# Optimization experiments

Measured on AMD Instinct MI355X. Metric: run time of the kernel, lower is better.

Reference implementation:

```python
import jax, jax.numpy as jnp
import numpy as np

# DeepSeek V4 MLA sparse attention dims
T = 512            # query tokens
H = 64             # attention heads (SUPPORTED_HEAD_COUNTS)
KV_LORA = 512      # kv_lora_rank (value dim = latent nope part)
ROPE = 64          # qk_rope_head_dim
D = KV_LORA + ROPE # 576 = head_dim (matches alignment=576 in cache spec)
N_KV = 8192        # cached compressed-KV tokens
TOPK = 1024        # top-k selected tokens per query
SCALE = 1.0 / np.sqrt(D).astype(np.float32)


def setup_inputs() -> dict:
    key = jax.random.key(0)
    k1, k2, k3, k4 = jax.random.split(key, 4)
    q = jax.random.normal(k1, (T, H, D), dtype=jnp.float32)
    kv = jax.random.normal(k2, (N_KV, D), dtype=jnp.float32)   # compressed KV latent cache (1 kv head)
    topk_idx = jax.random.randint(k3, (T, TOPK), 0, N_KV, dtype=jnp.int32)
    sink = jax.random.normal(k4, (H,), dtype=jnp.float32)       # per-head attention sink logit
    return {"q": q, "kv": kv, "topk_idx": topk_idx, "sink": sink}


def reference(q, kv, topk_idx, sink):
    # Sparse MLA: each query token attends only to its top-k latent cache slots.
    valid = topk_idx >= 0                       # invalid slots marked negative
    idx = jnp.maximum(topk_idx, 0)
    g = kv[idx]                                  # [T, K, D] gathered latents
    # scores over gathered subset: [T, H, K]
    scores = jnp.einsum('thd,tkd->thk', q, g) * SCALE
    scores = jnp.where(valid[:, None, :], scores, -jnp.inf)
    # sink-aware softmax: sink acts as an extra logit with zero value
    m = jnp.maximum(jnp.max(scores, axis=-1), sink[None, :])   # [T, H]
    p = jnp.exp(scores - m[..., None])                          # [T, H, K]
    denom = jnp.sum(p, axis=-1) + jnp.exp(sink[None, :] - m)    # [T, H]
    # value = nope part (first KV_LORA dims) of latent -> output [T, H, KV_LORA]
    out = jnp.einsum('thk,tkv->thv', p, g[..., :KV_LORA]) / denom[..., None]
    return out
```

## Files before the change

### kernel.cpp

```cpp
#include <hip/hip_runtime.h>
#include <hip/hip_bf16.h>

#define T_TOK 512
#define NH    64
#define HD    576
#define DVAL  512
#define NKV   8192
#define TOPK  1024
#define KT    32
#define NITER (TOPK / KT)
#define KSTEPS (HD / 32)
#define SCALE 0.041666666666666664f
#define LOG2E 1.4426950408889634f
#define QSCL  (SCALE * LOG2E)
#define MFIX  8.0f
#define MB    (MFIX * LOG2E)

typedef __attribute__((ext_vector_type(4))) float f32x4;
typedef __attribute__((ext_vector_type(8))) _Float16 half8;
typedef __attribute__((ext_vector_type(4))) unsigned short us4;
typedef __attribute__((ext_vector_type(8))) unsigned short us8;
typedef __attribute__((ext_vector_type(4))) int i32x4;

__device__ __forceinline__ unsigned short f2h(float x) {
    _Float16 h = (_Float16)x;
    return __builtin_bit_cast(unsigned short, h);
}

__device__ __forceinline__ float fexp2(float x) {
#if __has_builtin(__builtin_amdgcn_exp2f)
    return __builtin_amdgcn_exp2f(x);
#else
    return __expf(x * 0.6931471805599453f);
#endif
}

template<int CTRL>
__device__ __forceinline__ float dppmv(float x) {
    int r = __builtin_amdgcn_update_dpp(0, __builtin_bit_cast(int, x), CTRL, 0xF, 0xF, true);
    return __builtin_bit_cast(float, r);
}
__device__ __forceinline__ float red16sum(float x) {
    x += dppmv<0xB1>(x);
    x += dppmv<0x4E>(x);
    x += dppmv<0x141>(x);
    x += dppmv<0x140>(x);
    return x;
}

#define TICK_BARRIER() do {                                   \
    asm volatile("s_waitcnt lgkmcnt(0)" ::: "memory");        \
    __builtin_amdgcn_s_barrier();                             \
    asm volatile("" ::: "memory");                            \
} while (0)

__global__ void cvt_kv_f16(const float* __restrict__ kv, unsigned short* __restrict__ kvb) {
    int i = blockIdx.x * 256 + threadIdx.x;
    const f32x4* src = (const f32x4*)kv + (size_t)i * 2;
    f32x4 a = src[0];
    f32x4 b = src[1];
    us8 w;
    w[0]=f2h(a[0]); w[1]=f2h(a[1]); w[2]=f2h(a[2]); w[3]=f2h(a[3]);
    w[4]=f2h(b[0]); w[5]=f2h(b[1]); w[6]=f2h(b[2]); w[7]=f2h(b[3]);
    ((us8*)kvb)[i] = w;
}

#define G_LD  584
#define P_LD  40
#define GT_IDX(row,key) (((((row) << 5) | (key))) ^ ((((row) >> 2) & 7) << 3))

struct StageRegs { us8 v[4]; us4 rope; };

__device__ __forceinline__ void stage_load(
    const unsigned short* __restrict__ kvb, const int* __restrict__ tkrow,
    int it, int w8, int kg, int lm, int quad, int l16, StageRegs& R)
{
    const int* ip = tkrow + it * KT + kg * 4;
    i32x4 r4 = *(const i32x4*)ip;
    int d0 = w8 * 64 + lm * 8;
    #pragma unroll
    for (int j = 0; j < 4; j++) {
        int r = r4[j] < 0 ? 0 : r4[j];
        R.v[j] = *(const us8*)(kvb + (size_t)r * HD + d0);
    }
    int kr = tkrow[it * KT + w8 * 4 + quad];
    if (kr < 0) kr = 0;
    R.rope = *(const us4*)(kvb + (size_t)kr * HD + 512 + l16 * 4);
}

__device__ __forceinline__ void stage_write(
    int w8, int kg, int lm, int quad, int l16, const StageRegs& R,
    unsigned short (*gp)[G_LD], unsigned short* gtp)
{
    int d0 = w8 * 64 + lm * 8;
    #pragma unroll
    for (int j = 0; j < 4; j++)
        *(us8*)&gp[kg * 4 + j][d0] = R.v[j];
    #pragma unroll
    for (int e = 0; e < 8; e++) {
        us4 wv;
        wv[0] = R.v[0][e]; wv[1] = R.v[1][e]; wv[2] = R.v[2][e]; wv[3] = R.v[3][e];
        *(us4*)&gtp[GT_IDX(d0 + e, kg * 4)] = wv;
    }
    *(us4*)&gp[w8 * 4 + quad][512 + l16 * 4] = R.rope;
}

__global__ __launch_bounds__(1024, 4) void mla_sparse_kernel(
    const float* __restrict__ q, const int* __restrict__ topk,
    const float* __restrict__ sink, const unsigned short* __restrict__ kvb,
    float* __restrict__ out)
{
    __shared__ unsigned short g2[2][KT][G_LD];
    __shared__ unsigned short gtb[2][DVAL * KT];
    __shared__ unsigned short pbuf[2][NH][P_LD];
    __shared__ float lhalf[2][NH];

    const int t    = blockIdx.x;
    const int tid  = threadIdx.x;
    const int lane = tid & 63;
    const int quad = lane >> 4;
    const int l16  = lane & 15;
    const int wave = __builtin_amdgcn_readfirstlane(tid >> 6);
    const int* tkrow = topk + (size_t)t * TOPK;

    if (wave < 8) {
        const int hg = wave >> 1;
        const int kh = wave & 1;
        const int qo = quad * 8;
        const int krow0 = kh * 16;
        half8 qf[KSTEPS];
        {
            const float* qrow = q + ((size_t)t * NH + (hg * 16 + l16)) * HD;
            #pragma unroll
            for (int ks = 0; ks < KSTEPS; ks++) {
                int d0 = ks * 32 + qo;
                f32x4 a = *(const f32x4*)(qrow + d0);
                f32x4 b = *(const f32x4*)(qrow + d0 + 4);
                half8 h;
                h[0]=(_Float16)(a[0]*QSCL); h[1]=(_Float16)(a[1]*QSCL);
                h[2]=(_Float16)(a[2]*QSCL); h[3]=(_Float16)(a[3]*QSCL);
                h[4]=(_Float16)(b[0]*QSCL); h[5]=(_Float16)(b[1]*QSCL);
                h[6]=(_Float16)(b[2]*QSCL); h[7]=(_Float16)(b[3]*QSCL);
                qf[ks] = h;
            }
        }
        unsigned mbit = 0;
        #pragma unroll 4
        for (int kk = 0; kk < NITER; kk++)
            mbit |= (tkrow[kk * KT + krow0 + l16] < 0) ? (1u << kk) : 0u;
        f32x4 sk = *(const f32x4*)(sink + hg * 16 + quad * 4);
        float l_part[4];
        #pragma unroll
        for (int r = 0; r < 4; r++)
            l_part[r] = (kh == 0 && l16 == 0) ? fexp2(sk[r] * LOG2E - MB) : 0.0f;
        const int hb = hg * 16 + quad * 4;

        __syncthreads();

        for (int k = 0; k <= NITER; k++) {
            if (k < NITER) {
                const int par = k & 1;
                const unsigned short (*gp)[G_LD] = g2[par];
                f32x4 zero = {0.f, 0.f, 0.f, 0.f};
                f32x4 sa = zero, sb = zero;
                __builtin_amdgcn_s_setprio(1);
                #pragma unroll
                for (int ks = 0; ks < KSTEPS; ks += 2) {
                    half8 b0 = *(const half8*)&gp[krow0 + l16][ks * 32 + qo];
                    sa = __builtin_amdgcn_mfma_f32_16x16x32_f16(qf[ks], b0, sa, 0, 0, 0);
                    half8 b1 = *(const half8*)&gp[krow0 + l16][ks * 32 + 32 + qo];
                    sb = __builtin_amdgcn_mfma_f32_16x16x32_f16(qf[ks + 1], b1, sb, 0, 0, 0);
                }
                __builtin_amdgcn_s_setprio(0);
                f32x4 sacc = sa + sb;
                const bool bad = (mbit >> k) & 1;
                const float NEG = -__builtin_inff();
                #pragma unroll
                for (int r = 0; r < 4; r++) {
                    float v = bad ? NEG : sacc[r];
                    float p = fexp2(v - MB);
                    l_part[r] += p;
                    pbuf[par][hb + r][krow0 + l16] = f2h(p);
                }
            }
            TICK_BARRIER();
        }
        #pragma unroll
        for (int r = 0; r < 4; r++) l_part[r] = red16sum(l_part[r]);
        if (l16 == 0) {
            f32x4 l4; l4[0]=l_part[0]; l4[1]=l_part[1]; l4[2]=l_part[2]; l4[3]=l_part[3];
            *(f32x4*)&lhalf[kh][hb] = l4;
        }
        __syncthreads();
    } else {
        const int w8   = wave - 8;
        const int col0 = w8 * 64;
        const int kg   = lane >> 3;
        const int lm   = lane & 7;
        f32x4 acc[4][4];
        f32x4 zero = {0.f, 0.f, 0.f, 0.f};
        #pragma unroll
        for (int mt = 0; mt < 4; mt++)
            #pragma unroll
            for (int nt = 0; nt < 4; nt++) acc[mt][nt] = zero;

        {
            StageRegs R;
            stage_load(kvb, tkrow, 0, w8, kg, lm, quad, l16, R);
            stage_write(w8, kg, lm, quad, l16, R, g2[0], gtb[0]);
        }
        __syncthreads();

        for (int k = 0; k <= NITER; k++) {
            const int par = k & 1;
            StageRegs R;
            const bool do_stage = (k + 1) < NITER;
            if (do_stage)
                stage_load(kvb, tkrow, k + 1, w8, kg, lm, quad, l16, R);

            if (k >= 1) {
                const unsigned short (*pb)[P_LD] = pbuf[par ^ 1];
                const unsigned short* gtp = gtb[par ^ 1];
                half8 pa[4];
                #pragma unroll
                for (int mt = 0; mt < 4; mt++)
                    pa[mt] = *(const half8*)&pb[mt * 16 + l16][quad * 8];
                __builtin_amdgcn_s_setprio(1);
                #pragma unroll
                for (int nt = 0; nt < 4; nt++) {
                    half8 vb = *(const half8*)&gtp[GT_IDX(col0 + nt * 16 + l16, quad * 8)];
                    #pragma unroll
                    for (int mt = 0; mt < 4; mt++)
                        acc[mt][nt] = __builtin_amdgcn_mfma_f32_16x16x32_f16(pa[mt], vb, acc[mt][nt], 0, 0, 0);
                }
                __builtin_amdgcn_s_setprio(0);
            }
            if (do_stage) {
                asm volatile("s_waitcnt lgkmcnt(0)" ::: "memory");
                stage_write(w8, kg, lm, quad, l16, R, g2[par ^ 1], gtb[par ^ 1]);
            }
            TICK_BARRIER();
        }
        __syncthreads();

        #pragma unroll
        for (int mt = 0; mt < 4; mt++) {
            f32x4 lv0 = *(const f32x4*)&lhalf[0][mt * 16 + quad * 4];
            f32x4 lv1 = *(const f32x4*)&lhalf[1][mt * 16 + quad * 4];
            f32x4 li;
            li[0] = 1.0f / (lv0[0] + lv1[0]); li[1] = 1.0f / (lv0[1] + lv1[1]);
            li[2] = 1.0f / (lv0[2] + lv1[2]); li[3] = 1.0f / (lv0[3] + lv1[3]);
            #pragma unroll
            for (int nt = 0; nt < 4; nt++) {
                int vcol = col0 + nt * 16 + l16;
                f32x4 r = acc[mt][nt] * li;
                #pragma unroll
                for (int rr = 0; rr < 4; rr++) {
                    int head = mt * 16 + quad * 4 + rr;
                    out[((size_t)t * NH + head) * DVAL + vcol] = r[rr];
                }
            }
        }
    }
}

extern "C" void kernel_launch(void* const* d_in, const int* in_sizes, int n_in,
                              void* d_out, int out_size, void* d_ws, size_t ws_size,
                              hipStream_t stream) {
    const float* q    = (const float*)d_in[0];
    const float* kv   = (const float*)d_in[1];
    const int*   topk = (const int*)d_in[2];
    const float* sink = (const float*)d_in[3];
    float* out = (float*)d_out;
    unsigned short* kvb = (unsigned short*)d_ws;

    cvt_kv_f16<<<NKV * HD / (256 * 8), 256, 0, stream>>>(kv, kvb);
    mla_sparse_kernel<<<T_TOK, 1024, 0, stream>>>(q, topk, sink, kvb, out);
}
```

Before: 274.5 us.

## Load score-side KV fragments directly from global memory, drop row-major LDS stage

The score waves now fetch their B-operand KV rows straight from global/L2 into registers with a 4-deep software prefetch, removing the row-major LDS copy (g2) and the rope staging. Score waves are reduced from 8 to 4, each handling both 16-key halves, so the block shrinks to 768 threads and the split denominator merge is removed. This cuts LDS footprint and LDS write traffic, which may allow more blocks per CU. In exchange, score waves depend on global load latency and each KV row is read twice from cache, once for scores and once for the transposed value stage.

```diff
diff --git a/kernel.cpp b/kernel.cpp
--- a/kernel.cpp
+++ b/kernel.cpp
@@ -65,15 +65,14 @@
     ((us8*)kvb)[i] = w;
 }
 
-#define G_LD  584
-#define P_LD  40
+#define P_LD 40
 #define GT_IDX(row,key) (((((row) << 5) | (key))) ^ ((((row) >> 2) & 7) << 3))
 
-struct StageRegs { us8 v[4]; us4 rope; };
+struct StageRegs { us8 v[4]; };
 
 __device__ __forceinline__ void stage_load(
     const unsigned short* __restrict__ kvb, const int* __restrict__ tkrow,
-    int it, int w8, int kg, int lm, int quad, int l16, StageRegs& R)
+    int it, int w8, int kg, int lm, StageRegs& R)
 {
     const int* ip = tkrow + it * KT + kg * 4;
     i32x4 r4 = *(const i32x4*)ip;
@@ -83,37 +82,28 @@
         int r = r4[j] < 0 ? 0 : r4[j];
         R.v[j] = *(const us8*)(kvb + (size_t)r * HD + d0);
     }
-    int kr = tkrow[it * KT + w8 * 4 + quad];
-    if (kr < 0) kr = 0;
-    R.rope = *(const us4*)(kvb + (size_t)kr * HD + 512 + l16 * 4);
 }
 
 __device__ __forceinline__ void stage_write(
-    int w8, int kg, int lm, int quad, int l16, const StageRegs& R,
-    unsigned short (*gp)[G_LD], unsigned short* gtp)
+    int w8, int kg, int lm, const StageRegs& R, unsigned short* gtp)
 {
     int d0 = w8 * 64 + lm * 8;
-    #pragma unroll
-    for (int j = 0; j < 4; j++)
-        *(us8*)&gp[kg * 4 + j][d0] = R.v[j];
     #pragma unroll
     for (int e = 0; e < 8; e++) {
         us4 wv;
         wv[0] = R.v[0][e]; wv[1] = R.v[1][e]; wv[2] = R.v[2][e]; wv[3] = R.v[3][e];
         *(us4*)&gtp[GT_IDX(d0 + e, kg * 4)] = wv;
     }
-    *(us4*)&gp[w8 * 4 + quad][512 + l16 * 4] = R.rope;
-}
-
-__global__ __launch_bounds__(1024, 4) void mla_sparse_kernel(
+}
+
+__global__ __launch_bounds__(768, 3) void mla_sparse_kernel(
     const float* __restrict__ q, const int* __restrict__ topk,
     const float* __restrict__ sink, const unsigned short* __restrict__ kvb,
     float* __restrict__ out)
 {
-    __shared__ unsigned short g2[2][KT][G_LD];
     __shared__ unsigned short gtb[2][DVAL * KT];
     __shared__ unsigned short pbuf[2][NH][P_LD];
-    __shared__ float lhalf[2][NH];
+    __shared__ float lrunL[NH];
 
     const int t    = blockIdx.x;
     const int tid  = threadIdx.x;
@@ -123,14 +113,12 @@
     const int wave = __builtin_amdgcn_readfirstlane(tid >> 6);
     const int* tkrow = topk + (size_t)t * TOPK;
 
-    if (wave < 8) {
-        const int hg = wave >> 1;
-        const int kh = wave & 1;
+    if (wave < 4) {
+        const int w  = wave;
         const int qo = quad * 8;
-        const int krow0 = kh * 16;
         half8 qf[KSTEPS];
         {
-            const float* qrow = q + ((size_t)t * NH + (hg * 16 + l16)) * HD;
+            const float* qrow = q + ((size_t)t * NH + (w * 16 + l16)) * HD;
             #pragma unroll
             for (int ks = 0; ks < KSTEPS; ks++) {
                 int d0 = ks * 32 + qo;
@@ -144,43 +132,59 @@
                 qf[ks] = h;
             }
         }
-        unsigned mbit = 0;
+        unsigned mb0 = 0, mb1 = 0;
         #pragma unroll 4
-        for (int kk = 0; kk < NITER; kk++)
-            mbit |= (tkrow[kk * KT + krow0 + l16] < 0) ? (1u << kk) : 0u;
-        f32x4 sk = *(const f32x4*)(sink + hg * 16 + quad * 4);
+        for (int kk = 0; kk < NITER; kk++) {
+            mb0 |= (tkrow[kk * KT + l16]      < 0) ? (1u << kk) : 0u;
+            mb1 |= (tkrow[kk * KT + 16 + l16] < 0) ? (1u << kk) : 0u;
+        }
+        f32x4 sk = *(const f32x4*)(sink + w * 16 + quad * 4);
         float l_part[4];
         #pragma unroll
         for (int r = 0; r < 4; r++)
-            l_part[r] = (kh == 0 && l16 == 0) ? fexp2(sk[r] * LOG2E - MB) : 0.0f;
-        const int hb = hg * 16 + quad * 4;
+            l_part[r] = (l16 == 0) ? fexp2(sk[r] * LOG2E - MB) : 0.0f;
+        const int hb = w * 16 + quad * 4;
 
         __syncthreads();
 
         for (int k = 0; k <= NITER; k++) {
             if (k < NITER) {
                 const int par = k & 1;
-                const unsigned short (*gp)[G_LD] = g2[par];
-                f32x4 zero = {0.f, 0.f, 0.f, 0.f};
-                f32x4 sa = zero, sb = zero;
-                __builtin_amdgcn_s_setprio(1);
-                #pragma unroll
-                for (int ks = 0; ks < KSTEPS; ks += 2) {
-                    half8 b0 = *(const half8*)&gp[krow0 + l16][ks * 32 + qo];
-                    sa = __builtin_amdgcn_mfma_f32_16x16x32_f16(qf[ks], b0, sa, 0, 0, 0);
-                    half8 b1 = *(const half8*)&gp[krow0 + l16][ks * 32 + 32 + qo];
-                    sb = __builtin_amdgcn_mfma_f32_16x16x32_f16(qf[ks + 1], b1, sb, 0, 0, 0);
-                }
-                __builtin_amdgcn_s_setprio(0);
-                f32x4 sacc = sa + sb;
-                const bool bad = (mbit >> k) & 1;
+                int ra = tkrow[k * KT + l16];      ra = ra < 0 ? 0 : ra;
+                int rb = tkrow[k * KT + 16 + l16]; rb = rb < 0 ? 0 : rb;
+                const unsigned short* pA = kvb + (size_t)ra * HD + qo;
+                const unsigned short* pB = kvb + (size_t)rb * HD + qo;
+                half8 fa[4], fb[4];
+                #pragma unroll
+                for (int j = 0; j < 4; j++) {
+                    fa[j] = *(const half8*)(pA + j * 32);
+                    fb[j] = *(const half8*)(pB + j * 32);
+                }
+                f32x4 s0 = {0.f,0.f,0.f,0.f}, s1 = {0.f,0.f,0.f,0.f};
+                #pragma unroll
+                for (int ks = 0; ks < KSTEPS; ks++) {
+                    half8 ca = fa[ks & 3], cb = fb[ks & 3];
+                    if (ks + 4 < KSTEPS) {
+                        fa[ks & 3] = *(const half8*)(pA + (ks + 4) * 32);
+                        fb[ks & 3] = *(const half8*)(pB + (ks + 4) * 32);
+                    }
+                    __builtin_amdgcn_s_setprio(1);
+                    s0 = __builtin_amdgcn_mfma_f32_16x16x32_f16(qf[ks], ca, s0, 0, 0, 0);
+                    s1 = __builtin_amdgcn_mfma_f32_16x16x32_f16(qf[ks], cb, s1, 0, 0, 0);
+                    __builtin_amdgcn_s_setprio(0);
+                }
+                const bool bad0 = (mb0 >> k) & 1;
+                const bool bad1 = (mb1 >> k) & 1;
                 const float NEG = -__builtin_inff();
                 #pragma unroll
                 for (int r = 0; r < 4; r++) {
-                    float v = bad ? NEG : sacc[r];
-                    float p = fexp2(v - MB);
-                    l_part[r] += p;
-                    pbuf[par][hb + r][krow0 + l16] = f2h(p);
+                    float v0 = bad0 ? NEG : s0[r];
+                    float v1 = bad1 ? NEG : s1[r];
+                    float p0 = fexp2(v0 - MB);
+                    float p1 = fexp2(v1 - MB);
+                    l_part[r] += p0 + p1;
+                    pbuf[par][hb + r][l16]      = f2h(p0);
+                    pbuf[par][hb + r][16 + l16] = f2h(p1);
                 }
             }
             TICK_BARRIER();
@@ -189,11 +193,11 @@
         for (int r = 0; r < 4; r++) l_part[r] = red16sum(l_part[r]);
         if (l16 == 0) {
             f32x4 l4; l4[0]=l_part[0]; l4[1]=l_part[1]; l4[2]=l_part[2]; l4[3]=l_part[3];
-            *(f32x4*)&lhalf[kh][hb] = l4;
+            *(f32x4*)&lrunL[hb] = l4;
         }
         __syncthreads();
     } else {
-        const int w8   = wave - 8;
+        const int w8   = wave - 4;
         const int col0 = w8 * 64;
         const int kg   = lane >> 3;
         const int lm   = lane & 7;
@@ -206,8 +210,8 @@
 
         {
             StageRegs R;
-            stage_load(kvb, tkrow, 0, w8, kg, lm, quad, l16, R);
-            stage_write(w8, kg, lm, quad, l16, R, g2[0], gtb[0]);
+            stage_load(kvb, tkrow, 0, w8, kg, lm, R);
+            stage_write(w8, kg, lm, R, gtb[0]);
         }
         __syncthreads();
 
@@ -216,7 +220,7 @@
             StageRegs R;
             const bool do_stage = (k + 1) < NITER;
             if (do_stage)
-                stage_load(kvb, tkrow, k + 1, w8, kg, lm, quad, l16, R);
+                stage_load(kvb, tkrow, k + 1, w8, kg, lm, R);
 
             if (k >= 1) {
                 const unsigned short (*pb)[P_LD] = pbuf[par ^ 1];
@@ -237,7 +241,7 @@
             }
             if (do_stage) {
                 asm volatile("s_waitcnt lgkmcnt(0)" ::: "memory");
-                stage_write(w8, kg, lm, quad, l16, R, g2[par ^ 1], gtb[par ^ 1]);
+                stage_write(w8, kg, lm, R, gtb[par ^ 1]);
             }
             TICK_BARRIER();
         }
@@ -245,11 +249,10 @@
 
         #pragma unroll
         for (int mt = 0; mt < 4; mt++) {
-            f32x4 lv0 = *(const f32x4*)&lhalf[0][mt * 16 + quad * 4];
-            f32x4 lv1 = *(const f32x4*)&lhalf[1][mt * 16 + quad * 4];
+            f32x4 lv = *(const f32x4*)&lrunL[mt * 16 + quad * 4];
             f32x4 li;
-            li[0] = 1.0f / (lv0[0] + lv1[0]); li[1] = 1.0f / (lv0[1] + lv1[1]);
-            li[2] = 1.0f / (lv0[2] + lv1[2]); li[3] = 1.0f / (lv0[3] + lv1[3]);
+            li[0] = 1.0f / lv[0]; li[1] = 1.0f / lv[1];
+            li[2] = 1.0f / lv[2]; li[3] = 1.0f / lv[3];
             #pragma unroll
             for (int nt = 0; nt < 4; nt++) {
                 int vcol = col0 + nt * 16 + l16;
@@ -275,5 +278,5 @@
     unsigned short* kvb = (unsigned short*)d_ws;
 
     cvt_kv_f16<<<NKV * HD / (256 * 8), 256, 0, stream>>>(kv, kvb);
-    mla_sparse_kernel<<<T_TOK, 1024, 0, stream>>>(q, topk, sink, kvb, out);
-}
+    mla_sparse_kernel<<<T_TOK, 768, 0, stream>>>(q, topk, sink, kvb, out);
+}
```

After: 467.4 us. 70.2% more time.

## Halve score-producer waves by giving each two head groups sharing B fragments

Applied to the files above, without the earlier changes.

The score stage now uses 4 waves instead of 8. Each wave holds Q fragments for 32 heads and reuses every loaded KV B-fragment for two MFMAs. Block size drops from 1024 to 768 threads, which reduces LDS reads of the gathered KV and the number of waves per block. In exchange each score wave does twice the MFMA and exp work and holds more registers for Q, which may lengthen the score phase relative to the PV consumer waves.

```diff
diff --git a/kernel.cpp b/kernel.cpp
--- a/kernel.cpp
+++ b/kernel.cpp
@@ -105,7 +105,7 @@
     *(us4*)&gp[w8 * 4 + quad][512 + l16 * 4] = R.rope;
 }
 
-__global__ __launch_bounds__(1024, 4) void mla_sparse_kernel(
+__global__ __launch_bounds__(768, 3) void mla_sparse_kernel(
     const float* __restrict__ q, const int* __restrict__ topk,
     const float* __restrict__ sink, const unsigned short* __restrict__ kvb,
     float* __restrict__ out)
@@ -123,37 +123,50 @@
     const int wave = __builtin_amdgcn_readfirstlane(tid >> 6);
     const int* tkrow = topk + (size_t)t * TOPK;
 
-    if (wave < 8) {
-        const int hg = wave >> 1;
-        const int kh = wave & 1;
-        const int qo = quad * 8;
+    if (wave < 4) {
+        const int kh    = wave >> 1;
+        const int hg    = wave & 1;
         const int krow0 = kh * 16;
-        half8 qf[KSTEPS];
+        const int hbase = hg * 32;
+        const int qo    = quad * 8;
+        half8 qa[KSTEPS], qb[KSTEPS];
         {
-            const float* qrow = q + ((size_t)t * NH + (hg * 16 + l16)) * HD;
+            const float* qrowA = q + ((size_t)t * NH + (hbase + l16)) * HD;
+            const float* qrowB = q + ((size_t)t * NH + (hbase + 16 + l16)) * HD;
             #pragma unroll
             for (int ks = 0; ks < KSTEPS; ks++) {
                 int d0 = ks * 32 + qo;
-                f32x4 a = *(const f32x4*)(qrow + d0);
-                f32x4 b = *(const f32x4*)(qrow + d0 + 4);
-                half8 h;
-                h[0]=(_Float16)(a[0]*QSCL); h[1]=(_Float16)(a[1]*QSCL);
-                h[2]=(_Float16)(a[2]*QSCL); h[3]=(_Float16)(a[3]*QSCL);
-                h[4]=(_Float16)(b[0]*QSCL); h[5]=(_Float16)(b[1]*QSCL);
-                h[6]=(_Float16)(b[2]*QSCL); h[7]=(_Float16)(b[3]*QSCL);
-                qf[ks] = h;
-            }
-        }
-        unsigned mbit = 0;
+                f32x4 a0 = *(const f32x4*)(qrowA + d0);
+                f32x4 a1 = *(const f32x4*)(qrowA + d0 + 4);
+                f32x4 b0 = *(const f32x4*)(qrowB + d0);
+                f32x4 b1 = *(const f32x4*)(qrowB + d0 + 4);
+                half8 ha, hb;
+                ha[0]=(_Float16)(a0[0]*QSCL); ha[1]=(_Float16)(a0[1]*QSCL);
+                ha[2]=(_Float16)(a0[2]*QSCL); ha[3]=(_Float16)(a0[3]*QSCL);
+                ha[4]=(_Float16)(a1[0]*QSCL); ha[5]=(_Float16)(a1[1]*QSCL);
+                ha[6]=(_Float16)(a1[2]*QSCL); ha[7]=(_Float16)(a1[3]*QSCL);
+                hb[0]=(_Float16)(b0[0]*QSCL); hb[1]=(_Float16)(b0[1]*QSCL);
+                hb[2]=(_Float16)(b0[2]*QSCL); hb[3]=(_Float16)(b0[3]*QSCL);
+                hb[4]=(_Float16)(b1[0]*QSCL); hb[5]=(_Float16)(b1[1]*QSCL);
+                hb[6]=(_Float16)(b1[2]*QSCL); hb[7]=(_Float16)(b1[3]*QSCL);
+                qa[ks] = ha; qb[ks] = hb;
+            }
+        }
+        unsigned mb = 0;
         #pragma unroll 4
         for (int kk = 0; kk < NITER; kk++)
-            mbit |= (tkrow[kk * KT + krow0 + l16] < 0) ? (1u << kk) : 0u;
-        f32x4 sk = *(const f32x4*)(sink + hg * 16 + quad * 4);
-        float l_part[4];
-        #pragma unroll
-        for (int r = 0; r < 4; r++)
-            l_part[r] = (kh == 0 && l16 == 0) ? fexp2(sk[r] * LOG2E - MB) : 0.0f;
-        const int hb = hg * 16 + quad * 4;
+            mb |= (tkrow[kk * KT + krow0 + l16] < 0) ? (1u << kk) : 0u;
+        f32x4 skA = *(const f32x4*)(sink + hbase + quad * 4);
+        f32x4 skB = *(const f32x4*)(sink + hbase + 16 + quad * 4);
+        float lpA[4], lpB[4];
+        #pragma unroll
+        for (int r = 0; r < 4; r++) {
+            bool own = (kh == 0) && (l16 == 0);
+            lpA[r] = own ? fexp2(skA[r] * LOG2E - MB) : 0.0f;
+            lpB[r] = own ? fexp2(skB[r] * LOG2E - MB) : 0.0f;
+        }
+        const int hbA = hbase + quad * 4;
+        const int hbB = hbase + 16 + quad * 4;
 
         __syncthreads();
 
@@ -161,39 +174,42 @@
             if (k < NITER) {
                 const int par = k & 1;
                 const unsigned short (*gp)[G_LD] = g2[par];
-                f32x4 zero = {0.f, 0.f, 0.f, 0.f};
-                f32x4 sa = zero, sb = zero;
+                f32x4 s0 = {0.f,0.f,0.f,0.f}, s1 = {0.f,0.f,0.f,0.f};
                 __builtin_amdgcn_s_setprio(1);
                 #pragma unroll
-                for (int ks = 0; ks < KSTEPS; ks += 2) {
-                    half8 b0 = *(const half8*)&gp[krow0 + l16][ks * 32 + qo];
-                    sa = __builtin_amdgcn_mfma_f32_16x16x32_f16(qf[ks], b0, sa, 0, 0, 0);
-                    half8 b1 = *(const half8*)&gp[krow0 + l16][ks * 32 + 32 + qo];
-                    sb = __builtin_amdgcn_mfma_f32_16x16x32_f16(qf[ks + 1], b1, sb, 0, 0, 0);
+                for (int ks = 0; ks < KSTEPS; ks++) {
+                    half8 bf = *(const half8*)&gp[krow0 + l16][ks * 32 + qo];
+                    s0 = __builtin_amdgcn_mfma_f32_16x16x32_f16(qa[ks], bf, s0, 0, 0, 0);
+                    s1 = __builtin_amdgcn_mfma_f32_16x16x32_f16(qb[ks], bf, s1, 0, 0, 0);
                 }
                 __builtin_amdgcn_s_setprio(0);
-                f32x4 sacc = sa + sb;
-                const bool bad = (mbit >> k) & 1;
+                const bool bad = (mb >> k) & 1;
                 const float NEG = -__builtin_inff();
                 #pragma unroll
                 for (int r = 0; r < 4; r++) {
-                    float v = bad ? NEG : sacc[r];
-                    float p = fexp2(v - MB);
-                    l_part[r] += p;
-                    pbuf[par][hb + r][krow0 + l16] = f2h(p);
+                    float v0 = bad ? NEG : s0[r];
+                    float v1 = bad ? NEG : s1[r];
+                    float p0 = fexp2(v0 - MB);
+                    float p1 = fexp2(v1 - MB);
+                    lpA[r] += p0;
+                    lpB[r] += p1;
+                    pbuf[par][hbA + r][krow0 + l16] = f2h(p0);
+                    pbuf[par][hbB + r][krow0 + l16] = f2h(p1);
                 }
             }
             TICK_BARRIER();
         }
         #pragma unroll
-        for (int r = 0; r < 4; r++) l_part[r] = red16sum(l_part[r]);
+        for (int r = 0; r < 4; r++) { lpA[r] = red16sum(lpA[r]); lpB[r] = red16sum(lpB[r]); }
         if (l16 == 0) {
-            f32x4 l4; l4[0]=l_part[0]; l4[1]=l_part[1]; l4[2]=l_part[2]; l4[3]=l_part[3];
-            *(f32x4*)&lhalf[kh][hb] = l4;
+            f32x4 lA; lA[0]=lpA[0]; lA[1]=lpA[1]; lA[2]=lpA[2]; lA[3]=lpA[3];
+            f32x4 lB; lB[0]=lpB[0]; lB[1]=lpB[1]; lB[2]=lpB[2]; lB[3]=lpB[3];
+            *(f32x4*)&lhalf[kh][hbA] = lA;
+            *(f32x4*)&lhalf[kh][hbB] = lB;
         }
         __syncthreads();
     } else {
-        const int w8   = wave - 8;
+        const int w8   = wave - 4;
         const int col0 = w8 * 64;
         const int kg   = lane >> 3;
         const int lm   = lane & 7;
@@ -275,5 +291,5 @@
     unsigned short* kvb = (unsigned short*)d_ws;
 
     cvt_kv_f16<<<NKV * HD / (256 * 8), 256, 0, stream>>>(kv, kvb);
-    mla_sparse_kernel<<<T_TOK, 1024, 0, stream>>>(q, topk, sink, kvb, out);
-}
+    mla_sparse_kernel<<<T_TOK, 768, 0, stream>>>(q, topk, sink, kvb, out);
+}
```

After: 371.0 us. 35.1% more time.
